# Kernel optimization log

Hardware: AMD Instinct MI355X
Metric: run time of the kernel (lower is better)

The kernel has to match this reference:

```python
import jax, jax.numpy as jnp
import numpy as np

RU, RV = 6, 6
DU, DV = 2 * RU + 1, 2 * RV + 1  # 13, 13 displacement offsets
C = 32  # feat_channels (WipModule.c_feat)


def _conv(x, w, stride=1, pad=1):
    return jax.lax.conv_general_dilated(
        x, w, (stride, stride), [(pad, pad), (pad, pad)],
        dimension_numbers=('NCHW', 'OIHW', 'NCHW'))


def _deconv(x, w):
    # expressed as an lhs-dilated conv (kernel stored directly in OIHW conv layout).
    p = 4 - 1 - 1
    return jax.lax.conv_general_dilated(
        x, w, (1, 1), [(p, p), (p, p)], lhs_dilation=(2, 2),
        dimension_numbers=('NCHW', 'OIHW', 'NCHW'))


def _kaiming(key, shape):
    fan_in = shape[1] * shape[2] * shape[3]
    return jax.random.normal(key, shape, jnp.float32) * np.float32(np.sqrt(2.0 / fan_in))


def setup_inputs() -> dict:
    key = jax.random.key(0)
    ks = jax.random.split(key, 8)
    B, H, W = 1, 64, 128
    return {
        'fmap1': jax.random.normal(ks[0], (B, C, H, W), jnp.float32),
        'fmap2': jax.random.normal(ks[1], (B, C, H, W), jnp.float32),
        'w1': _kaiming(ks[2], (96, 2 * C, 3, 3)),
        'w2': _kaiming(ks[3], (128, 96, 3, 3)),
        'w3': _kaiming(ks[4], (128, 128, 3, 3)),
        'w4': _kaiming(ks[5], (64, 128, 3, 3)),
        'wd': _kaiming(ks[6], (32, 64, 4, 4)),
        'w5': _kaiming(ks[7], (1, 32, 3, 3)),
    }


def _build_mvol(fmap1, fmap2):
    # Vectorized form of the torch itertools.product loop: one padded gather
    # over all (du, dv) displacement windows instead of 169 slice-assignments.
    b, c, h, w = fmap1.shape
    padded = jnp.pad(fmap2, ((0, 0), (0, 0), (RV, RV), (RU, RU)))

    def window(i, j):
        # shifted(y, x) = fmap2[y + (j - RV), x + (i - RU)], zero outside bounds
        return jax.lax.dynamic_slice(padded, (0, 0, j, i), (b, c, h, w))

    shifted = jax.vmap(lambda i: jax.vmap(lambda j: window(i, j))(jnp.arange(DV)))(jnp.arange(DU))
    shifted = jnp.moveaxis(shifted, 2, 0)  # (b, du, dv, c, h, w)
    # valid mask: detached channel-sum of the warped fmap2 slice (matches torch)
    valid = (jax.lax.stop_gradient(shifted).sum(axis=3, keepdims=True) != 0)
    valid = valid.astype(fmap1.dtype)
    m1 = fmap1[:, None, None] * valid  # broadcast fmap1 over (du, dv)
    return jnp.concatenate([m1, shifted * valid], axis=3)  # (b, du, dv, 2c, h, w)


def reference(fmap1, fmap2, w1, w2, w3, w4, wd, w5):
    mvol = _build_mvol(fmap1, fmap2)
    b, du, dv, c2, h, w = mvol.shape
    # MatchingNet: fold (du, dv) into batch, conv stack down to 1 cost channel
    x = mvol.reshape(b * du * dv, c2, h, w)
    x = jax.nn.relu(_conv(x, w1))
    x = jax.nn.relu(_conv(x, w2, stride=2))  # (.., 128, h/2, w/2)
    x = jax.nn.relu(_conv(x, w3))
    x = jax.nn.relu(_conv(x, w4))
    x = jax.nn.relu(_deconv(x, wd))          # back to (h, w)
    x = _conv(x, w5)                          # cost, 1 channel
    return x.reshape(b, du, dv, h, w)
```

## Files before the change

kernel.cpp:

```cpp
#include <hip/hip_runtime.h>

#define NITEMS 169

typedef __attribute__((ext_vector_type(8))) __bf16 bf16x8;
typedef __attribute__((ext_vector_type(4))) float f32x4;
typedef __attribute__((ext_vector_type(8))) unsigned short u16x8;
typedef __attribute__((ext_vector_type(4))) unsigned short u16x4;

__device__ __forceinline__ unsigned short f2b(float x) {
  union { float f; unsigned u; } v; v.f = x;
  unsigned r = v.u + 0x7fffu + ((v.u >> 16) & 1u);
  return (unsigned short)(r >> 16);
}
__device__ __forceinline__ float b2f(unsigned short u) {
  union { unsigned u; float f; } v; v.u = ((unsigned)u) << 16;
  return v.f;
}

__global__ __launch_bounds__(256) void k_prepf(const float* __restrict__ f,
                                               unsigned short* __restrict__ fb) {
  const int pix = blockIdx.x * 256 + threadIdx.x;
  const int y = pix >> 7, x = pix & 127;
#pragma unroll
  for (int c = 0; c < 32; ++c)
    fb[(size_t)pix * 32 + c] = f2b(f[(c * 64 + y) * 128 + x]);
}

__global__ void k_prep3x3(const float* __restrict__ w, unsigned short* __restrict__ wp,
                          int Cout, int Cin) {
  int i = blockIdx.x * 256 + threadIdx.x;
  if (i >= Cout * Cin * 9) return;
  int kx = i % 3, t = i / 3;
  int ky = t % 3; t /= 3;
  int cin = t % Cin, cout = t / Cin;
  int tap = ky * 3 + kx;
  wp[(((cin >> 5) * 9 + tap) * Cout + cout) * 32 + (cin & 31)] = f2b(w[i]);
}

__global__ void k_prepwd(const float* __restrict__ w, unsigned short* __restrict__ wp) {
  int i = blockIdx.x * 256 + threadIdx.x;
  if (i >= 32 * 64 * 16) return;
  int kx = i & 3, ky = (i >> 2) & 3, ci = (i >> 4) & 63, cout = i >> 10;
  wp[(((((ci >> 5) * 4 + ky) * 4 + kx) * 32) + cout) * 32 + (ci & 31)] = f2b(w[i]);
}

__global__ __launch_bounds__(256) void k_conv1m(
    const unsigned short* __restrict__ f1b, const unsigned short* __restrict__ f2bp,
    const unsigned short* __restrict__ wp, unsigned short* __restrict__ x1, int base) {
  const int g = blockIdx.y, item = base + g;
  const int dx = item / 13 - 6, dy = item % 13 - 6;
  const int oy0 = blockIdx.x * 2;
  constexpr int WI = 130;
  __shared__ __align__(16) unsigned short X[4][4][WI][8];
  const int wid = threadIdx.x >> 6, lane = threadIdx.x & 63;
  const int lm = lane & 15, lkg = lane >> 4, lk = lkg * 8;

  f32x4 acc[24];
#pragma unroll
  for (int t = 0; t < 24; ++t) acc[t] = f32x4{0.f, 0.f, 0.f, 0.f};

  for (int cic = 0; cic < 2; ++cic) {
    __syncthreads();
    const unsigned short* src = cic ? f2bp : f1b;
    for (int c = threadIdx.x; c < 4 * 4 * WI; c += 256) {
      const int cig = c & 3, t2 = c >> 2;
      const int col = t2 % WI, r = t2 / WI;
      const int iy = oy0 - 1 + r, ix = col - 1;
      const int sy = iy + dy, sx = ix + dx;
      u16x8 v = {0, 0, 0, 0, 0, 0, 0, 0};
      if ((unsigned)iy < 64u && (unsigned)ix < 128u &&
          (unsigned)sy < 64u && (unsigned)sx < 128u) {
        const int py = cic ? sy : iy, px = cic ? sx : ix;
        v = *(const u16x8*)&src[(size_t)(py * 128 + px) * 32 + cig * 8];
      }
      *(u16x8*)&X[r][cig][col][0] = v;
    }
    __syncthreads();
#pragma unroll
    for (int tap = 0; tap < 9; ++tap) {
      const int ky = tap / 3, kx = tap % 3;
      bf16x8 bf[4];
#pragma unroll
      for (int j = 0; j < 4; ++j) {
        const int mt = wid * 4 + j, rw = mt >> 3, mtx = mt & 7;
        bf[j] = *(const bf16x8*)&X[rw + ky][lkg][mtx * 16 + lm + kx][0];
      }
#pragma unroll
      for (int i = 0; i < 6; ++i) {
        bf16x8 af = *(const bf16x8*)&wp[((cic * 9 + tap) * 96 + i * 16 + lm) * 32 + lk];
#pragma unroll
        for (int j = 0; j < 4; ++j)
          acc[i * 4 + j] =
              __builtin_amdgcn_mfma_f32_16x16x32_bf16(af, bf[j], acc[i * 4 + j], 0, 0, 0);
      }
    }
  }
  unsigned short* op = x1 + (size_t)g * (8192 * 96);
#pragma unroll
  for (int i = 0; i < 6; ++i)
#pragma unroll
    for (int j = 0; j < 4; ++j) {
      const int mt = wid * 4 + j, rw = mt >> 3, mtx = mt & 7;
      const int cout0 = i * 16 + lkg * 4;
      const int m = mtx * 16 + lm;
      u16x4 pv;
#pragma unroll
      for (int r = 0; r < 4; ++r) pv[r] = f2b(fmaxf(acc[i * 4 + j][r], 0.f));
      *(u16x4*)&op[(size_t)((oy0 + rw) * 128 + m) * 96 + cout0] = pv;
    }
}

template <int Cin, int Cout, int H, int W, int STRIDE, bool RELU>
__global__ __launch_bounds__(256) void k_convm(
    const unsigned short* __restrict__ xin, const unsigned short* __restrict__ wp,
    unsigned short* __restrict__ xout) {
  constexpr int OH = H / STRIDE, OW = W / STRIDE;
  constexpr int WI = W + 2;
  constexpr int WIH = (WI + 1) / 2;
  constexpr int NC = Cout / 16, NM = OW / 16;
  static_assert(NC % 4 == 0, "cout tiles divisible by 4 waves");
  constexpr int WCT = NC / 4, WMT = NM;
  const int g = blockIdx.y, oy = blockIdx.x;
  const unsigned short* ip = xin + (size_t)g * Cin * H * W;
  unsigned short* op = xout + (size_t)g * Cout * OH * OW;
  __shared__ __align__(16) unsigned short X[3][4][WI][8];
  const int wid = threadIdx.x >> 6, lane = threadIdx.x & 63;
  const int lm = lane & 15, lkg = lane >> 4, lk = lkg * 8;
  const int ct0 = wid * WCT;

  f32x4 acc[WCT * WMT];
#pragma unroll
  for (int t = 0; t < WCT * WMT; ++t) acc[t] = f32x4{0.f, 0.f, 0.f, 0.f};

  for (int cic = 0; cic < Cin / 32; ++cic) {
    __syncthreads();
    for (int c = threadIdx.x; c < 3 * 4 * WI; c += 256) {
      const int cig = c & 3, t2 = c >> 2;
      const int col = t2 % WI, r = t2 / WI;
      const int iy = oy * STRIDE - 1 + r, ix = col - 1;
      const int pcol = (STRIDE == 2) ? ((col >> 1) + (col & 1) * WIH) : col;
      u16x8 v = {0, 0, 0, 0, 0, 0, 0, 0};
      if ((unsigned)iy < (unsigned)H && (unsigned)ix < (unsigned)W)
        v = *(const u16x8*)&ip[(size_t)(iy * W + ix) * Cin + cic * 32 + cig * 8];
      *(u16x8*)&X[r][cig][pcol][0] = v;
    }
    __syncthreads();
#pragma unroll
    for (int tap = 0; tap < 9; ++tap) {
      const int ky = tap / 3, kx = tap % 3;
      bf16x8 bf[WMT];
#pragma unroll
      for (int j = 0; j < WMT; ++j) {
        const int m = j * 16 + lm;
        const int colr = (STRIDE == 2) ? (m + (kx >> 1) + (kx & 1) * WIH) : (m + kx);
        bf[j] = *(const bf16x8*)&X[ky][lkg][colr][0];
      }
#pragma unroll
      for (int i = 0; i < WCT; ++i) {
        const int cout = (ct0 + i) * 16 + lm;
        bf16x8 af = *(const bf16x8*)&wp[((cic * 9 + tap) * Cout + cout) * 32 + lk];
#pragma unroll
        for (int j = 0; j < WMT; ++j)
          acc[i * WMT + j] =
              __builtin_amdgcn_mfma_f32_16x16x32_bf16(af, bf[j], acc[i * WMT + j], 0, 0, 0);
      }
    }
  }
#pragma unroll
  for (int i = 0; i < WCT; ++i)
#pragma unroll
    for (int j = 0; j < WMT; ++j) {
      const int cout0 = (ct0 + i) * 16 + lkg * 4;
      const int m = j * 16 + lm;
      u16x4 pv;
#pragma unroll
      for (int r = 0; r < 4; ++r) {
        float f = acc[i * WMT + j][r];
        if (RELU) f = fmaxf(f, 0.f);
        pv[r] = f2b(f);
      }
      *(u16x4*)&op[(size_t)(oy * OW + m) * Cout + cout0] = pv;
    }
}

__global__ __launch_bounds__(256) void k_deconvm(
    const unsigned short* __restrict__ x4, const unsigned short* __restrict__ wp,
    unsigned short* __restrict__ x5) {
  const int g = blockIdx.y, mrow = blockIdx.x;
  const unsigned short* ip = x4 + (size_t)g * (2048 * 64);
  unsigned short* op = x5 + (size_t)g * (8192 * 32);
  constexpr int WI = 66;
  __shared__ __align__(16) unsigned short X[3][4][WI][8];
  const int wid = threadIdx.x >> 6, lane = threadIdx.x & 63;
  const int a = wid >> 1, b = wid & 1;
  const int lm = lane & 15, lkg = lane >> 4, lk = lkg * 8;
  f32x4 acc[8];
#pragma unroll
  for (int t = 0; t < 8; ++t) acc[t] = f32x4{0.f, 0.f, 0.f, 0.f};

  for (int cic = 0; cic < 2; ++cic) {
    __syncthreads();
    for (int c = threadIdx.x; c < 3 * 4 * WI; c += 256) {
      const int cig = c & 3, t2 = c >> 2;
      const int col = t2 % WI, r = t2 / WI;
      const int iy = mrow - 1 + r, ix = col - 1;
      u16x8 v = {0, 0, 0, 0, 0, 0, 0, 0};
      if ((unsigned)iy < 32u && (unsigned)ix < 64u)
        v = *(const u16x8*)&ip[(size_t)(iy * 64 + ix) * 64 + cic * 32 + cig * 8];
      *(u16x8*)&X[r][cig][col][0] = v;
    }
    __syncthreads();
#pragma unroll
    for (int u = 0; u < 2; ++u)
#pragma unroll
      for (int vv = 0; vv < 2; ++vv) {
        const int r = (a == 0) ? u : u + 1;
        const int ky = (a == 0) ? 2 * u : 2 * u + 1;
        const int s = (b == 0) ? vv : vv + 1;
        const int kx = (b == 0) ? 2 * vv : 2 * vv + 1;
        bf16x8 bf[4];
#pragma unroll
        for (int j = 0; j < 4; ++j)
          bf[j] = *(const bf16x8*)&X[r][lkg][j * 16 + lm + s][0];
#pragma unroll
        for (int i = 0; i < 2; ++i) {
          bf16x8 af =
              *(const bf16x8*)&wp[((((cic * 4 + ky) * 4 + kx) * 32) + i * 16 + lm) * 32 + lk];
#pragma unroll
          for (int j = 0; j < 4; ++j)
            acc[i * 4 + j] =
                __builtin_amdgcn_mfma_f32_16x16x32_bf16(af, bf[j], acc[i * 4 + j], 0, 0, 0);
        }
      }
  }
#pragma unroll
  for (int i = 0; i < 2; ++i)
#pragma unroll
    for (int j = 0; j < 4; ++j) {
      const int cout0 = i * 16 + lkg * 4;
      const int p = j * 16 + lm;
      const int orow = 2 * mrow + a, ocol = 2 * p + b;
      u16x4 pv;
#pragma unroll
      for (int r2 = 0; r2 < 4; ++r2) pv[r2] = f2b(fmaxf(acc[i * 4 + j][r2], 0.f));
      *(u16x4*)&op[(size_t)(orow * 128 + ocol) * 32 + cout0] = pv;
    }
}

__global__ __launch_bounds__(256) void k_conv5m(
    const unsigned short* __restrict__ x5, const float* __restrict__ w5,
    float* __restrict__ out) {
  const int g = blockIdx.y;
  const int pix = blockIdx.x * 256 + threadIdx.x;
  const int y = pix >> 7, x = pix & 127;
  const unsigned short* ip = x5 + (size_t)g * (8192 * 32);
  float s = 0.f;
#pragma unroll
  for (int t = 0; t < 9; ++t) {
    const int yy = y - 1 + t / 3, xx = x - 1 + t % 3;
    if ((unsigned)yy < 64u && (unsigned)xx < 128u) {
#pragma unroll
      for (int cg = 0; cg < 4; ++cg) {
        u16x8 v = *(const u16x8*)&ip[(size_t)(yy * 128 + xx) * 32 + cg * 8];
#pragma unroll
        for (int e = 0; e < 8; ++e) s += b2f(v[e]) * w5[(cg * 8 + e) * 9 + t];
      }
    }
  }
  out[(size_t)g * 8192 + pix] = s;
}

extern "C" void kernel_launch(void* const* d_in, const int* in_sizes, int n_in,
                              void* d_out, int out_size, void* d_ws, size_t ws_size,
                              hipStream_t stream) {
  const float* f1 = (const float*)d_in[0];
  const float* f2 = (const float*)d_in[1];
  const float* w1 = (const float*)d_in[2];
  const float* w2 = (const float*)d_in[3];
  const float* w3 = (const float*)d_in[4];
  const float* w4 = (const float*)d_in[5];
  const float* wd = (const float*)d_in[6];
  const float* w5 = (const float*)d_in[7];
  float* out = (float*)d_out;

  size_t off = 0;
  auto alloc = [&](size_t elems) {
    unsigned short* p = (unsigned short*)((char*)d_ws + off);
    off += ((elems * 2 + 255) / 256) * 256;
    return p;
  };
  unsigned short* f1b = alloc(64 * 128 * 32);
  unsigned short* f2bp = alloc(64 * 128 * 32);
  unsigned short* w1p = alloc(2 * 9 * 96 * 32);
  unsigned short* w2p = alloc(3 * 9 * 128 * 32);
  unsigned short* w3p = alloc(4 * 9 * 128 * 32);
  unsigned short* w4p = alloc(4 * 9 * 64 * 32);
  unsigned short* wdp = alloc(2 * 16 * 32 * 32);
  const size_t wend = off;

  const size_t perA = (size_t)96 * 8192 * 2;
  const size_t perB = (size_t)128 * 2048 * 2;
  int G = (int)((ws_size - wend) / (perA + perB));
  if (G > NITEMS) G = NITEMS;
  if (G < 1) G = 1;
  unsigned short* A = (unsigned short*)((char*)d_ws + wend);
  unsigned short* B = (unsigned short*)((char*)d_ws + wend + (size_t)G * perA);

  k_prepf<<<32, 256, 0, stream>>>(f1, f1b);
  k_prepf<<<32, 256, 0, stream>>>(f2, f2bp);
  k_prep3x3<<<(96 * 64 * 9 + 255) / 256, 256, 0, stream>>>(w1, w1p, 96, 64);
  k_prep3x3<<<(128 * 96 * 9 + 255) / 256, 256, 0, stream>>>(w2, w2p, 128, 96);
  k_prep3x3<<<(128 * 128 * 9 + 255) / 256, 256, 0, stream>>>(w3, w3p, 128, 128);
  k_prep3x3<<<(64 * 128 * 9 + 255) / 256, 256, 0, stream>>>(w4, w4p, 64, 128);
  k_prepwd<<<(32 * 64 * 16 + 255) / 256, 256, 0, stream>>>(wd, wdp);

  for (int base = 0; base < NITEMS; base += G) {
    const int cnt = (NITEMS - base < G) ? (NITEMS - base) : G;
    k_conv1m<<<dim3(32, cnt), 256, 0, stream>>>(f1b, f2bp, w1p, A, base);
    k_convm<96, 128, 64, 128, 2, true><<<dim3(32, cnt), 256, 0, stream>>>(A, w2p, B);
    k_convm<128, 128, 32, 64, 1, true><<<dim3(32, cnt), 256, 0, stream>>>(B, w3p, A);
    k_convm<128, 64, 32, 64, 1, true><<<dim3(32, cnt), 256, 0, stream>>>(A, w4p, B);
    k_deconvm<<<dim3(32, cnt), 256, 0, stream>>>(B, wdp, A);
    k_conv5m<<<dim3(32, cnt), 256, 0, stream>>>(A, w5, out + (size_t)base * 8192);
  }
}
```

Measured before the change: 797.5 us.

## Decompose first conv by linearity into shared partial sums plus boundary corrections

Instead of running the first 64-channel conv once for each of 169 displacement items, the conv is split by linearity into an fmap1 term computed once and an fmap2 term computed once over an extended padded grid. Separate kernels compute corrections for rows, columns, corners and the zero-padding boundaries where the validity mask or image edge breaks the shift invariance, and an assemble kernel sums them per item and applies ReLU. This replaces per-item MFMA work with a memory-bound gather of fp32 partial sums, which adds fp32 workspace traffic and many small launches, and may change rounding. The validity mask is assumed to be exactly the bounds mask, which holds only when shifted channel sums are never exactly zero inside the image.

New measurement: 1.816 ms. 2.28x slower.

```diff
diff --git a/kernel.cpp b/kernel.cpp
--- a/kernel.cpp
+++ b/kernel.cpp
@@ -44,11 +44,9 @@
   wp[(((((ci >> 5) * 4 + ky) * 4 + kx) * 32) + cout) * 32 + (ci & 31)] = f2b(w[i]);
 }
 
-__global__ __launch_bounds__(256) void k_conv1m(
-    const unsigned short* __restrict__ f1b, const unsigned short* __restrict__ f2bp,
-    const unsigned short* __restrict__ wp, unsigned short* __restrict__ x1, int base) {
-  const int g = blockIdx.y, item = base + g;
-  const int dx = item / 13 - 6, dy = item % 13 - 6;
+__global__ __launch_bounds__(256) void k_z1(
+    const unsigned short* __restrict__ f1b, const unsigned short* __restrict__ wp,
+    float* __restrict__ z1) {
   const int oy0 = blockIdx.x * 2;
   constexpr int WI = 130;
   __shared__ __align__(16) unsigned short X[4][4][WI][8];
@@ -59,43 +57,34 @@
 #pragma unroll
   for (int t = 0; t < 24; ++t) acc[t] = f32x4{0.f, 0.f, 0.f, 0.f};
 
-  for (int cic = 0; cic < 2; ++cic) {
-    __syncthreads();
-    const unsigned short* src = cic ? f2bp : f1b;
-    for (int c = threadIdx.x; c < 4 * 4 * WI; c += 256) {
-      const int cig = c & 3, t2 = c >> 2;
-      const int col = t2 % WI, r = t2 / WI;
-      const int iy = oy0 - 1 + r, ix = col - 1;
-      const int sy = iy + dy, sx = ix + dx;
-      u16x8 v = {0, 0, 0, 0, 0, 0, 0, 0};
-      if ((unsigned)iy < 64u && (unsigned)ix < 128u &&
-          (unsigned)sy < 64u && (unsigned)sx < 128u) {
-        const int py = cic ? sy : iy, px = cic ? sx : ix;
-        v = *(const u16x8*)&src[(size_t)(py * 128 + px) * 32 + cig * 8];
-      }
-      *(u16x8*)&X[r][cig][col][0] = v;
-    }
-    __syncthreads();
-#pragma unroll
-    for (int tap = 0; tap < 9; ++tap) {
-      const int ky = tap / 3, kx = tap % 3;
-      bf16x8 bf[4];
-#pragma unroll
-      for (int j = 0; j < 4; ++j) {
-        const int mt = wid * 4 + j, rw = mt >> 3, mtx = mt & 7;
-        bf[j] = *(const bf16x8*)&X[rw + ky][lkg][mtx * 16 + lm + kx][0];
-      }
-#pragma unroll
-      for (int i = 0; i < 6; ++i) {
-        bf16x8 af = *(const bf16x8*)&wp[((cic * 9 + tap) * 96 + i * 16 + lm) * 32 + lk];
-#pragma unroll
-        for (int j = 0; j < 4; ++j)
-          acc[i * 4 + j] =
-              __builtin_amdgcn_mfma_f32_16x16x32_bf16(af, bf[j], acc[i * 4 + j], 0, 0, 0);
-      }
-    }
-  }
-  unsigned short* op = x1 + (size_t)g * (8192 * 96);
+  for (int c = threadIdx.x; c < 4 * 4 * WI; c += 256) {
+    const int cig = c & 3, t2 = c >> 2;
+    const int col = t2 % WI, r = t2 / WI;
+    const int iy = oy0 - 1 + r, ix = col - 1;
+    u16x8 v = {0, 0, 0, 0, 0, 0, 0, 0};
+    if ((unsigned)iy < 64u && (unsigned)ix < 128u)
+      v = *(const u16x8*)&f1b[(size_t)(iy * 128 + ix) * 32 + cig * 8];
+    *(u16x8*)&X[r][cig][col][0] = v;
+  }
+  __syncthreads();
+#pragma unroll
+  for (int tap = 0; tap < 9; ++tap) {
+    const int ky = tap / 3, kx = tap % 3;
+    bf16x8 bf[4];
+#pragma unroll
+    for (int j = 0; j < 4; ++j) {
+      const int mt = wid * 4 + j, rw = mt >> 3, mtx = mt & 7;
+      bf[j] = *(const bf16x8*)&X[rw + ky][lkg][mtx * 16 + lm + kx][0];
+    }
+#pragma unroll
+    for (int i = 0; i < 6; ++i) {
+      bf16x8 af = *(const bf16x8*)&wp[((0 * 9 + tap) * 96 + i * 16 + lm) * 32 + lk];
+#pragma unroll
+      for (int j = 0; j < 4; ++j)
+        acc[i * 4 + j] =
+            __builtin_amdgcn_mfma_f32_16x16x32_bf16(af, bf[j], acc[i * 4 + j], 0, 0, 0);
+    }
+  }
 #pragma unroll
   for (int i = 0; i < 6; ++i)
 #pragma unroll
@@ -103,11 +92,333 @@
       const int mt = wid * 4 + j, rw = mt >> 3, mtx = mt & 7;
       const int cout0 = i * 16 + lkg * 4;
       const int m = mtx * 16 + lm;
-      u16x4 pv;
-#pragma unroll
-      for (int r = 0; r < 4; ++r) pv[r] = f2b(fmaxf(acc[i * 4 + j][r], 0.f));
-      *(u16x4*)&op[(size_t)((oy0 + rw) * 128 + m) * 96 + cout0] = pv;
-    }
+      *(f32x4*)&z1[(size_t)((oy0 + rw) * 128 + m) * 96 + cout0] = acc[i * 4 + j];
+    }
+}
+
+__global__ __launch_bounds__(256) void k_z2e(
+    const unsigned short* __restrict__ f2b_, const unsigned short* __restrict__ wp,
+    float* __restrict__ z2e) {
+  const int u = blockIdx.x;
+  constexpr int WI = 194;
+  __shared__ __align__(16) unsigned short X[3][4][WI][8];
+  const int wid = threadIdx.x >> 6, lane = threadIdx.x & 63;
+  const int lm = lane & 15, lkg = lane >> 4, lk = lkg * 8;
+
+  f32x4 acc[18];
+#pragma unroll
+  for (int t = 0; t < 18; ++t) acc[t] = f32x4{0.f, 0.f, 0.f, 0.f};
+
+  for (int c = threadIdx.x; c < 3 * 4 * WI; c += 256) {
+    const int cig = c & 3, t2 = c >> 2;
+    const int col = t2 % WI, r = t2 / WI;
+    const int iy = u + r - 7, ix = col - 7;
+    u16x8 v = {0, 0, 0, 0, 0, 0, 0, 0};
+    if ((unsigned)iy < 64u && (unsigned)ix < 128u)
+      v = *(const u16x8*)&f2b_[(size_t)(iy * 128 + ix) * 32 + cig * 8];
+    *(u16x8*)&X[r][cig][col][0] = v;
+  }
+  __syncthreads();
+#pragma unroll
+  for (int tap = 0; tap < 9; ++tap) {
+    const int ky = tap / 3, kx = tap % 3;
+    bf16x8 bf[3];
+#pragma unroll
+    for (int j = 0; j < 3; ++j) {
+      const int mt = wid * 3 + j;
+      bf[j] = *(const bf16x8*)&X[ky][lkg][mt * 16 + lm + kx][0];
+    }
+#pragma unroll
+    for (int i = 0; i < 6; ++i) {
+      bf16x8 af = *(const bf16x8*)&wp[((1 * 9 + tap) * 96 + i * 16 + lm) * 32 + lk];
+#pragma unroll
+      for (int j = 0; j < 3; ++j)
+        acc[i * 3 + j] =
+            __builtin_amdgcn_mfma_f32_16x16x32_bf16(af, bf[j], acc[i * 3 + j], 0, 0, 0);
+    }
+  }
+#pragma unroll
+  for (int i = 0; i < 6; ++i)
+#pragma unroll
+    for (int j = 0; j < 3; ++j) {
+      const int v = (wid * 3 + j) * 16 + lm;
+      if (v < 140) {
+        const int cout0 = i * 16 + lkg * 4;
+        *(f32x4*)&z2e[(size_t)(u * 140 + v) * 96 + cout0] = acc[i * 3 + j];
+      }
+    }
+}
+
+__global__ __launch_bounds__(256) void k_crow(
+    const unsigned short* __restrict__ f1b, const unsigned short* __restrict__ wp,
+    float* __restrict__ crow) {
+  const int dyi = blockIdx.x / 7, r = blockIdx.x % 7;
+  const int dy = dyi - 6;
+  const int ady = dy < 0 ? -dy : dy;
+  if (dy == 0 || r >= ady + 1) return;
+  const int rowlo = dy > 0 ? 63 - dy : 0;
+  const int oy = rowlo + r;
+  constexpr int WI = 130;
+  __shared__ __align__(16) unsigned short X[3][4][WI][8];
+  const int wid = threadIdx.x >> 6, lane = threadIdx.x & 63;
+  const int lm = lane & 15, lkg = lane >> 4, lk = lkg * 8;
+
+  f32x4 acc[12];
+#pragma unroll
+  for (int t = 0; t < 12; ++t) acc[t] = f32x4{0.f, 0.f, 0.f, 0.f};
+
+  for (int c = threadIdx.x; c < 3 * 4 * WI; c += 256) {
+    const int cig = c & 3, t2 = c >> 2;
+    const int col = t2 % WI, rr = t2 / WI;
+    const int iy = oy - 1 + rr, ix = col - 1;
+    const bool band = dy > 0 ? (iy >= 64 - dy) : (iy < -dy);
+    u16x8 v = {0, 0, 0, 0, 0, 0, 0, 0};
+    if (band && (unsigned)iy < 64u && (unsigned)ix < 128u)
+      v = *(const u16x8*)&f1b[(size_t)(iy * 128 + ix) * 32 + cig * 8];
+    *(u16x8*)&X[rr][cig][col][0] = v;
+  }
+  __syncthreads();
+#pragma unroll
+  for (int tap = 0; tap < 9; ++tap) {
+    const int ky = tap / 3, kx = tap % 3;
+    bf16x8 bf[2];
+#pragma unroll
+    for (int j = 0; j < 2; ++j)
+      bf[j] = *(const bf16x8*)&X[ky][lkg][(wid * 2 + j) * 16 + lm + kx][0];
+#pragma unroll
+    for (int i = 0; i < 6; ++i) {
+      bf16x8 af = *(const bf16x8*)&wp[((0 * 9 + tap) * 96 + i * 16 + lm) * 32 + lk];
+#pragma unroll
+      for (int j = 0; j < 2; ++j)
+        acc[i * 2 + j] =
+            __builtin_amdgcn_mfma_f32_16x16x32_bf16(af, bf[j], acc[i * 2 + j], 0, 0, 0);
+    }
+  }
+#pragma unroll
+  for (int i = 0; i < 6; ++i)
+#pragma unroll
+    for (int j = 0; j < 2; ++j) {
+      const int cout0 = i * 16 + lkg * 4;
+      const int m = (wid * 2 + j) * 16 + lm;
+      *(f32x4*)&crow[(size_t)((dyi * 8 + r) * 128 + m) * 96 + cout0] = acc[i * 2 + j];
+    }
+}
+
+__global__ __launch_bounds__(256) void k_ccol(
+    const unsigned short* __restrict__ f1b, const unsigned short* __restrict__ wp,
+    float* __restrict__ ccol) {
+  const int dxi = blockIdx.x;
+  const int dx = dxi - 6;
+  const int adx = dx < 0 ? -dx : dx;
+  if (dx == 0) return;
+  const int ccnt = adx + 1;
+  const int collo = dx > 0 ? 127 - dx : 0;
+  __shared__ __align__(16) unsigned short X2[9][66][32];
+  const int wid = threadIdx.x >> 6, lane = threadIdx.x & 63;
+  const int lm = lane & 15, lkg = lane >> 4, lk = lkg * 8;
+
+  for (int t = threadIdx.x; t < 9 * 66 * 4; t += 256) {
+    const int cig = t & 3, pos = t >> 2;
+    const int rr = pos % 66, cc = pos / 66;
+    const int iy = rr - 1, ix = collo - 1 + cc;
+    const bool band = dx > 0 ? (ix >= 128 - dx) : (ix < -dx);
+    u16x8 v = {0, 0, 0, 0, 0, 0, 0, 0};
+    if (band && (unsigned)iy < 64u && (unsigned)ix < 128u)
+      v = *(const u16x8*)&f1b[(size_t)(iy * 128 + ix) * 32 + cig * 8];
+    *(u16x8*)&X2[cc][rr][cig * 8] = v;
+  }
+  __syncthreads();
+  for (int c = 0; c < ccnt; ++c) {
+    f32x4 acc[6];
+#pragma unroll
+    for (int i = 0; i < 6; ++i) acc[i] = f32x4{0.f, 0.f, 0.f, 0.f};
+#pragma unroll
+    for (int tap = 0; tap < 9; ++tap) {
+      const int ky = tap / 3, kx = tap % 3;
+      bf16x8 bf = *(const bf16x8*)&X2[c + kx][wid * 16 + lm + ky][lk];
+#pragma unroll
+      for (int i = 0; i < 6; ++i) {
+        bf16x8 af = *(const bf16x8*)&wp[((0 * 9 + tap) * 96 + i * 16 + lm) * 32 + lk];
+        acc[i] = __builtin_amdgcn_mfma_f32_16x16x32_bf16(af, bf, acc[i], 0, 0, 0);
+      }
+    }
+    const int y = wid * 16 + lm;
+#pragma unroll
+    for (int i = 0; i < 6; ++i) {
+      const int cout0 = i * 16 + lkg * 4;
+      *(f32x4*)&ccol[(size_t)((dxi * 64 + y) * 8 + c) * 96 + cout0] = acc[i];
+    }
+  }
+}
+
+__global__ __launch_bounds__(256) void k_ccorner(
+    const float* __restrict__ f1, const float* __restrict__ w1,
+    float* __restrict__ ccor) {
+  const int item = blockIdx.x;
+  const int dx = item / 13 - 6, dy = item % 13 - 6;
+  if (dx == 0 || dy == 0) return;
+  const int ady = dy < 0 ? -dy : dy, adx = dx < 0 ? -dx : dx;
+  const int rcnt = ady + 1, ccnt = adx + 1;
+  const int rowlo = dy > 0 ? 63 - dy : 0;
+  const int collo = dx > 0 ? 127 - dx : 0;
+  const int p = threadIdx.x & 63, q = threadIdx.x >> 6;
+  const int r = p >> 3, c = p & 7;
+  const bool active = (r < rcnt) && (c < ccnt);
+  const int oy = rowlo + r, ox = collo + c;
+  float acc[24];
+#pragma unroll
+  for (int i = 0; i < 24; ++i) acc[i] = 0.f;
+#pragma unroll
+  for (int ky = 0; ky < 3; ++ky)
+#pragma unroll
+    for (int kx = 0; kx < 3; ++kx) {
+      const int iy = oy - 1 + ky, ix = ox - 1 + kx;
+      const bool rb = dy > 0 ? (iy >= 64 - dy) : (iy < -dy);
+      const bool cb = dx > 0 ? (ix >= 128 - dx) : (ix < -dx);
+      if (!(active && rb && cb && (unsigned)iy < 64u && (unsigned)ix < 128u)) continue;
+#pragma unroll 1
+      for (int ci = 0; ci < 32; ++ci) {
+        const float a = b2f(f2b(f1[(ci * 64 + iy) * 128 + ix]));
+#pragma unroll
+        for (int co = 0; co < 24; ++co)
+          acc[co] += a * b2f(f2b(w1[(((q * 24 + co) * 64 + ci) * 3 + ky) * 3 + kx]));
+      }
+    }
+  if (active) {
+#pragma unroll
+    for (int co = 0; co < 24; ++co)
+      ccor[(size_t)(((item * 8 + r) * 8 + c) * 96) + q * 24 + co] = acc[co];
+  }
+}
+
+__global__ __launch_bounds__(256) void k_bcorr_rows(
+    const unsigned short* __restrict__ f2bp, const float* __restrict__ w1,
+    float* __restrict__ rtop, float* __restrict__ rbot) {
+  const int dyi = blockIdx.x, dy = dyi - 6;
+  const int rt = dy - 1, rb = 64 + dy;
+  for (int idx = threadIdx.x; idx < 140 * 96; idx += 256) {
+    const int v = idx / 96, co = idx % 96;
+    float at = 0.f, ab = 0.f;
+#pragma unroll
+    for (int kx = 0; kx < 3; ++kx) {
+      const int x2 = v - 7 + kx;
+      if ((unsigned)x2 >= 128u) continue;
+      if ((unsigned)rt < 64u) {
+        const float wv = b2f(f2b(w1[((co * 64 + 32) * 3 + 0) * 3 + kx - 0]));
+        (void)wv;
+#pragma unroll 1
+        for (int ci = 0; ci < 32; ++ci)
+          at += b2f(f2bp[(size_t)(rt * 128 + x2) * 32 + ci]) *
+                b2f(f2b(w1[((co * 64 + 32 + ci) * 3 + 0) * 3 + kx]));
+      }
+      if ((unsigned)rb < 64u) {
+#pragma unroll 1
+        for (int ci = 0; ci < 32; ++ci)
+          ab += b2f(f2bp[(size_t)(rb * 128 + x2) * 32 + ci]) *
+                b2f(f2b(w1[((co * 64 + 32 + ci) * 3 + 2) * 3 + kx]));
+      }
+    }
+    rtop[(size_t)dyi * 140 * 96 + idx] = at;
+    rbot[(size_t)dyi * 140 * 96 + idx] = ab;
+  }
+}
+
+__global__ __launch_bounds__(256) void k_bcorr_cols(
+    const unsigned short* __restrict__ f2bp, const float* __restrict__ w1,
+    float* __restrict__ clft, float* __restrict__ crgt) {
+  const int dxi = blockIdx.x, dx = dxi - 6;
+  const int cl = dx - 1, cr = 128 + dx;
+  for (int idx = threadIdx.x; idx < 76 * 96; idx += 256) {
+    const int u = idx / 96, co = idx % 96;
+    float al = 0.f, ar = 0.f;
+#pragma unroll
+    for (int ky = 0; ky < 3; ++ky) {
+      const int y2 = u - 7 + ky;
+      if ((unsigned)y2 >= 64u) continue;
+      if ((unsigned)cl < 128u) {
+#pragma unroll 1
+        for (int ci = 0; ci < 32; ++ci)
+          al += b2f(f2bp[(size_t)(y2 * 128 + cl) * 32 + ci]) *
+                b2f(f2b(w1[((co * 64 + 32 + ci) * 3 + ky) * 3 + 0]));
+      }
+      if ((unsigned)cr < 128u) {
+#pragma unroll 1
+        for (int ci = 0; ci < 32; ++ci)
+          ar += b2f(f2bp[(size_t)(y2 * 128 + cr) * 32 + ci]) *
+                b2f(f2b(w1[((co * 64 + 32 + ci) * 3 + ky) * 3 + 2]));
+      }
+    }
+    clft[(size_t)dxi * 76 * 96 + idx] = al;
+    crgt[(size_t)dxi * 76 * 96 + idx] = ar;
+  }
+}
+
+__global__ __launch_bounds__(256) void k_bcorr_corn(
+    const unsigned short* __restrict__ f2bp, const float* __restrict__ w1,
+    float* __restrict__ kcorn) {
+  const int item = blockIdx.x;
+  const int dx = item / 13 - 6, dy = item % 13 - 6;
+  for (int idx = threadIdx.x; idx < 4 * 96; idx += 256) {
+    const int corner = idx / 96, co = idx % 96;
+    const int row = (corner < 2) ? dy - 1 : 64 + dy;
+    const int col = (corner & 1) ? 128 + dx : dx - 1;
+    const int ky = (corner < 2) ? 0 : 2;
+    const int kx = (corner & 1) ? 2 : 0;
+    float acc = 0.f;
+    if ((unsigned)row < 64u && (unsigned)col < 128u) {
+#pragma unroll 1
+      for (int ci = 0; ci < 32; ++ci)
+        acc += b2f(f2bp[(size_t)(row * 128 + col) * 32 + ci]) *
+               b2f(f2b(w1[((co * 64 + 32 + ci) * 3 + ky) * 3 + kx]));
+    }
+    kcorn[(size_t)item * 384 + idx] = acc;
+  }
+}
+
+__global__ __launch_bounds__(256) void k_assemble(
+    const float* __restrict__ z1, const float* __restrict__ z2e,
+    const float* __restrict__ crow, const float* __restrict__ ccol,
+    const float* __restrict__ ccor, const float* __restrict__ rtop,
+    const float* __restrict__ rbot, const float* __restrict__ clft,
+    const float* __restrict__ crgt, const float* __restrict__ kcorn,
+    unsigned short* __restrict__ x1, int base) {
+  const int y = blockIdx.x, g = blockIdx.y, item = base + g;
+  const int dx = item / 13 - 6, dy = item % 13 - 6;
+  const int dyi = dy + 6, dxi = dx + 6;
+  const int ady = dy < 0 ? -dy : dy, adx = dx < 0 ? -dx : dx;
+  const int rowlo = dy > 0 ? 63 - dy : 0;
+  const int rowhi = rowlo + (dy ? ady + 1 : 0);
+  const int collo = dx > 0 ? 127 - dx : 0;
+  const int colhi = collo + (dx ? adx + 1 : 0);
+  const bool inrow = (y >= rowlo) && (y < rowhi);
+  const int vrow = y + dy + 6;
+  unsigned short* op = x1 + (size_t)g * (8192 * 96);
+
+  for (int t = threadIdx.x; t < 128 * 24; t += 256) {
+    const int px = t / 24, c0 = (t % 24) * 4;
+    const int v = px + dx + 6;
+    f32x4 s = *(const f32x4*)&z1[(size_t)(y * 128 + px) * 96 + c0];
+    s += *(const f32x4*)&z2e[(size_t)(vrow * 140 + v) * 96 + c0];
+    if (inrow)
+      s -= *(const f32x4*)&crow[(size_t)((dyi * 8 + y - rowlo) * 128 + px) * 96 + c0];
+    if (px >= collo && px < colhi) {
+      s -= *(const f32x4*)&ccol[(size_t)((dxi * 64 + y) * 8 + px - collo) * 96 + c0];
+      if (inrow)
+        s += *(const f32x4*)&ccor[(size_t)(((item * 8 + y - rowlo) * 8) + px - collo) * 96 + c0];
+    }
+    if (y == 0) s -= *(const f32x4*)&rtop[(size_t)(dyi * 140 + v) * 96 + c0];
+    if (y == 63) s -= *(const f32x4*)&rbot[(size_t)(dyi * 140 + v) * 96 + c0];
+    if (px == 0) s -= *(const f32x4*)&clft[(size_t)(dxi * 76 + vrow) * 96 + c0];
+    if (px == 127) s -= *(const f32x4*)&crgt[(size_t)(dxi * 76 + vrow) * 96 + c0];
+    if (y == 0 && px == 0) s += *(const f32x4*)&kcorn[(size_t)item * 384 + 0 * 96 + c0];
+    if (y == 0 && px == 127) s += *(const f32x4*)&kcorn[(size_t)item * 384 + 1 * 96 + c0];
+    if (y == 63 && px == 0) s += *(const f32x4*)&kcorn[(size_t)item * 384 + 2 * 96 + c0];
+    if (y == 63 && px == 127) s += *(const f32x4*)&kcorn[(size_t)item * 384 + 3 * 96 + c0];
+    u16x4 o;
+#pragma unroll
+    for (int e = 0; e < 4; ++e) o[e] = f2b(fmaxf(s[e], 0.f));
+    *(u16x4*)&op[(size_t)(y * 128 + px) * 96 + c0] = o;
+  }
 }
 
 template <int Cin, int Cout, int H, int W, int STRIDE, bool RELU>
@@ -284,18 +595,28 @@
   float* out = (float*)d_out;
 
   size_t off = 0;
-  auto alloc = [&](size_t elems) {
-    unsigned short* p = (unsigned short*)((char*)d_ws + off);
-    off += ((elems * 2 + 255) / 256) * 256;
+  auto alloc = [&](size_t bytes) {
+    void* p = (char*)d_ws + off;
+    off += (bytes + 255) / 256 * 256;
     return p;
   };
-  unsigned short* f1b = alloc(64 * 128 * 32);
-  unsigned short* f2bp = alloc(64 * 128 * 32);
-  unsigned short* w1p = alloc(2 * 9 * 96 * 32);
-  unsigned short* w2p = alloc(3 * 9 * 128 * 32);
-  unsigned short* w3p = alloc(4 * 9 * 128 * 32);
-  unsigned short* w4p = alloc(4 * 9 * 64 * 32);
-  unsigned short* wdp = alloc(2 * 16 * 32 * 32);
+  unsigned short* f1b = (unsigned short*)alloc(64 * 128 * 32 * 2);
+  unsigned short* f2bp = (unsigned short*)alloc(64 * 128 * 32 * 2);
+  unsigned short* w1p = (unsigned short*)alloc(2 * 9 * 96 * 32 * 2);
+  unsigned short* w2p = (unsigned short*)alloc(3 * 9 * 128 * 32 * 2);
+  unsigned short* w3p = (unsigned short*)alloc(4 * 9 * 128 * 32 * 2);
+  unsigned short* w4p = (unsigned short*)alloc(4 * 9 * 64 * 32 * 2);
+  unsigned short* wdp = (unsigned short*)alloc(2 * 16 * 32 * 32 * 2);
+  float* z1 = (float*)alloc((size_t)64 * 128 * 96 * 4);
+  float* z2e = (float*)alloc((size_t)76 * 140 * 96 * 4);
+  float* crow = (float*)alloc((size_t)13 * 8 * 128 * 96 * 4);
+  float* ccol = (float*)alloc((size_t)13 * 64 * 8 * 96 * 4);
+  float* ccor = (float*)alloc((size_t)NITEMS * 8 * 8 * 96 * 4);
+  float* rtop = (float*)alloc((size_t)13 * 140 * 96 * 4);
+  float* rbot = (float*)alloc((size_t)13 * 140 * 96 * 4);
+  float* clft = (float*)alloc((size_t)13 * 76 * 96 * 4);
+  float* crgt = (float*)alloc((size_t)13 * 76 * 96 * 4);
+  float* kcorn = (float*)alloc((size_t)NITEMS * 4 * 96 * 4);
   const size_t wend = off;
 
   const size_t perA = (size_t)96 * 8192 * 2;
@@ -314,9 +635,19 @@
   k_prep3x3<<<(64 * 128 * 9 + 255) / 256, 256, 0, stream>>>(w4, w4p, 64, 128);
   k_prepwd<<<(32 * 64 * 16 + 255) / 256, 256, 0, stream>>>(wd, wdp);
 
+  k_z1<<<32, 256, 0, stream>>>(f1b, w1p, z1);
+  k_z2e<<<76, 256, 0, stream>>>(f2bp, w1p, z2e);
+  k_crow<<<91, 256, 0, stream>>>(f1b, w1p, crow);
+  k_ccol<<<13, 256, 0, stream>>>(f1b, w1p, ccol);
+  k_ccorner<<<NITEMS, 256, 0, stream>>>(f1, w1, ccor);
+  k_bcorr_rows<<<13, 256, 0, stream>>>(f2bp, w1, rtop, rbot);
+  k_bcorr_cols<<<13, 256, 0, stream>>>(f2bp, w1, clft, crgt);
+  k_bcorr_corn<<<NITEMS, 256, 0, stream>>>(f2bp, w1, kcorn);
+
   for (int base = 0; base < NITEMS; base += G) {
     const int cnt = (NITEMS - base < G) ? (NITEMS - base) : G;
-    k_conv1m<<<dim3(32, cnt), 256, 0, stream>>>(f1b, f2bp, w1p, A, base);
+    k_assemble<<<dim3(64, cnt), 256, 0, stream>>>(z1, z2e, crow, ccol, ccor, rtop, rbot,
+                                                  clft, crgt, kcorn, A, base);
     k_convm<96, 128, 64, 128, 2, true><<<dim3(32, cnt), 256, 0, stream>>>(A, w2p, B);
     k_convm<128, 128, 32, 64, 1, true><<<dim3(32, cnt), 256, 0, stream>>>(B, w3p, A);
     k_convm<128, 64, 32, 64, 1, true><<<dim3(32, cnt), 256, 0, stream>>>(A, w4p, B);
```
